# Optimization experiments

Measured on AMD Instinct MI355X. Metric: run time of the kernel, lower is better.

## Reference

```python
import jax, jax.numpy as jnp
import numpy as np

B, C_IN, L = 8, 64, 4096
C_OUT, HEADS = 64, 3
E = 524288
T_DIM = 256
N = B * L
EPS = 1e-5
NEG_SLOPE = 0.2  # PyG GATConv default negative_slope


def setup_inputs() -> dict:
    key = jax.random.key(0)
    ks = jax.random.split(key, 12)
    x = jax.random.normal(ks[0], (B, C_IN, L), jnp.float32)
    time_emb = jax.random.normal(ks[1], (B, T_DIM), jnp.float32)
    edge_index = jax.random.randint(ks[2], (2, E), 0, N, dtype=jnp.int32)
    # GATConv params: lin maps in -> heads*out; att_src/att_dst per head
    W_lin = jax.random.normal(ks[3], (C_IN, HEADS * C_OUT), jnp.float32) / np.sqrt(C_IN)
    att_src = jax.random.normal(ks[4], (1, HEADS, C_OUT), jnp.float32) / np.sqrt(C_OUT)
    att_dst = jax.random.normal(ks[5], (1, HEADS, C_OUT), jnp.float32) / np.sqrt(C_OUT)
    bias = jnp.zeros((C_OUT,), jnp.float32)
    # time projection (computed but unused in the source forward)
    tp_W = jax.random.normal(ks[6], (T_DIM, C_OUT), jnp.float32) / np.sqrt(T_DIM)
    tp_b = jnp.zeros((C_OUT,), jnp.float32)
    # BatchNorm1d affine params (training-mode batch stats)
    gamma = jnp.ones((C_OUT,), jnp.float32)
    beta = jnp.zeros((C_OUT,), jnp.float32)
    return {"x": x, "time_emb": time_emb, "edge_index": edge_index,
            "W_lin": W_lin, "att_src": att_src, "att_dst": att_dst,
            "bias": bias, "tp_W": tp_W, "tp_b": tp_b,
            "gamma": gamma, "beta": beta}


def reference(x, time_emb, edge_index, W_lin, att_src, att_dst, bias, tp_W, tp_b, gamma, beta):
    b, c, l = x.shape
    n = b * l
    # time projection: present in source but its result is never used
    _t = (time_emb @ tp_W + tp_b)[:, :, None]  # [b, C_OUT, 1] (dead)
    h = (x.reshape(-1, c) @ W_lin).reshape(n, HEADS, C_OUT)  # [N,H,C]
    a_src = (h * att_src).sum(-1)  # [N,H]
    a_dst = (h * att_dst).sum(-1)  # [N,H]
    # add self loops (PyG default add_self_loops=True)
    loops = jnp.arange(n, dtype=edge_index.dtype)
    src = jnp.concatenate([edge_index[0], loops])
    dst = jnp.concatenate([edge_index[1], loops])
    e = a_src[src] + a_dst[dst]                        # [E+N, H]
    e = jnp.where(e > 0, e, NEG_SLOPE * e)             # LeakyReLU
    emax = jax.ops.segment_max(e, dst, num_segments=n)  # every node has a self loop
    ex = jnp.exp(e - emax[dst])
    denom = jax.ops.segment_sum(ex, dst, num_segments=n)
    alpha = ex / denom[dst]                            # segment softmax over dst
    msg = alpha[:, :, None] * h[src]                   # [E+N, H, C]
    out = jax.ops.segment_sum(msg, dst, num_segments=n)  # [N,H,C]
    out = out.mean(axis=1) + bias                      # concat=False -> head mean
    # BatchNorm1d (training mode: biased batch stats)
    mu = out.mean(axis=0)
    var = ((out - mu) ** 2).mean(axis=0)
    out = (out - mu) / jnp.sqrt(var + EPS) * gamma + beta
    out = jax.nn.relu(out)
    return out.reshape(b, -1, l)
```

## Files before the change

### kernel.cpp

```cpp
#include <hip/hip_runtime.h>
#include <hip/hip_bf16.h>

#define N_NODES 32768
#define E_EDGES 524288
#define HC 192
#define NEG_SLOPE 0.2f
#define BN_EPS 1e-5f
#define PAD 64

typedef _Float16 f16;
typedef __attribute__((ext_vector_type(8))) _Float16 v8h;
typedef __attribute__((ext_vector_type(4))) float    v4f;

#define GEMM_BLOCKS 512
#define SCAT_BLOCKS 2048
#define FUSED_BLOCKS (GEMM_BLOCKS + SCAT_BLOCKS)

__device__ __forceinline__ float lrelu(float v) { return v > 0.f ? v : NEG_SLOPE * v; }

__device__ __forceinline__ float wave_sum(float v) {
#pragma unroll
    for (int off = 32; off > 0; off >>= 1) v += __shfl_xor(v, off);
    return v;
}
__device__ __forceinline__ float rlane(float v, int l) {
    return __uint_as_float(__builtin_amdgcn_readlane(__float_as_uint(v), l));
}

__global__ __launch_bounds__(256, 2) void k_fused(
        const int* __restrict__ esrc, const int* __restrict__ edst,
        int* __restrict__ cnt, unsigned short* __restrict__ csr_pad,
        const float* __restrict__ x, const float* __restrict__ W,
        const float* __restrict__ att_s, const float* __restrict__ att_d,
        f16* __restrict__ hh, float* __restrict__ a_src, float* __restrict__ a_dst,
        float* __restrict__ gp1, float* __restrict__ gp2) {
    if (blockIdx.x >= GEMM_BLOCKS) {
        int i = (blockIdx.x - GEMM_BLOCKS) * 256 + threadIdx.x;
        int s = esrc[i];
        int d = edst[i];
        int p = atomicAdd(&cnt[d], 1);
        if (p < PAD) csr_pad[d * PAD + p] = (unsigned short)s;
        return;
    }
    if (blockIdx.x == 0) {
        float4 z = make_float4(0.f, 0.f, 0.f, 0.f);
#pragma unroll
        for (int i2 = 0; i2 < 4; i2++) {
            ((float4*)gp1)[threadIdx.x * 4 + i2] = z;
            ((float4*)gp2)[threadIdx.x * 4 + i2] = z;
        }
    }
    const int lane = threadIdx.x & 63;
    const int wid  = (blockIdx.x * 256 + threadIdx.x) >> 6;
    const int q    = lane >> 4;
    const int nl   = lane & 15;
    const int n0   = wid * 16;

    v8h xf0, xf1;
    {
        const float* xr = x + (size_t)(n0 + nl) * 64 + q * 8;
        float4 lo = *(const float4*)(xr);
        float4 hi = *(const float4*)(xr + 4);
        xf0[0] = (f16)lo.x; xf0[1] = (f16)lo.y; xf0[2] = (f16)lo.z; xf0[3] = (f16)lo.w;
        xf0[4] = (f16)hi.x; xf0[5] = (f16)hi.y; xf0[6] = (f16)hi.z; xf0[7] = (f16)hi.w;
        lo = *(const float4*)(xr + 32);
        hi = *(const float4*)(xr + 36);
        xf1[0] = (f16)lo.x; xf1[1] = (f16)lo.y; xf1[2] = (f16)lo.z; xf1[3] = (f16)lo.w;
        xf1[4] = (f16)hi.x; xf1[5] = (f16)hi.y; xf1[6] = (f16)hi.z; xf1[7] = (f16)hi.w;
    }

    float sAcc = 0.f, dAcc = 0.f;
#pragma unroll
    for (int ct = 0; ct < 12; ct++) {
        const int c = ct * 16 + nl;
        v8h wf0, wf1;
#pragma unroll
        for (int j = 0; j < 8; j++) {
            wf0[j] = (f16)W[(q * 8 + j) * HC + c];
            wf1[j] = (f16)W[(32 + q * 8 + j) * HC + c];
        }
        float4 av = *(const float4*)(att_s + ct * 16 + q * 4);
        float4 dv = *(const float4*)(att_d + ct * 16 + q * 4);

        v4f C = {0.f, 0.f, 0.f, 0.f};
        C = __builtin_amdgcn_mfma_f32_16x16x32_f16(wf0, xf0, C, 0, 0, 0);
        C = __builtin_amdgcn_mfma_f32_16x16x32_f16(wf1, xf1, C, 0, 0, 0);

        union { f16 h[4]; unsigned long long u; } pk;
        pk.h[0] = (f16)C[0]; pk.h[1] = (f16)C[1];
        pk.h[2] = (f16)C[2]; pk.h[3] = (f16)C[3];
        *(unsigned long long*)(hh + (size_t)(n0 + nl) * HC + ct * 16 + q * 4) = pk.u;

        sAcc = fmaf(C[0], av.x, sAcc); sAcc = fmaf(C[1], av.y, sAcc);
        sAcc = fmaf(C[2], av.z, sAcc); sAcc = fmaf(C[3], av.w, sAcc);
        dAcc = fmaf(C[0], dv.x, dAcc); dAcc = fmaf(C[1], dv.y, dAcc);
        dAcc = fmaf(C[2], dv.z, dAcc); dAcc = fmaf(C[3], dv.w, dAcc);

        if ((ct & 3) == 3) {
            float s = sAcc; s += __shfl_xor(s, 16); s += __shfl_xor(s, 32);
            float d = dAcc; d += __shfl_xor(d, 16); d += __shfl_xor(d, 32);
            if (lane < 16) {
                a_src[(n0 + lane) * 4 + (ct >> 2)] = s;
                a_dst[(n0 + lane) * 4 + (ct >> 2)] = d;
            }
            sAcc = 0.f; dAcc = 0.f;
        }
    }
}

__global__ __launch_bounds__(256, 4) void k_node(
        const f16* __restrict__ hh,
        const float* __restrict__ a_src,
        const float* __restrict__ a_dst,
        const int* __restrict__ cnt,
        const unsigned short* __restrict__ csr_pad,
        const float* __restrict__ bias,
        float* __restrict__ out_pre,
        float* __restrict__ gp1,
        float* __restrict__ gp2) {
    const int lane = threadIdx.x & 63;
    const int wv = threadIdx.x >> 6;
    const int n = blockIdx.x * 4 + wv;

    int deg = cnt[n]; if (deg > PAD) deg = PAD;
    const unsigned short* __restrict__ row = csr_pad + n * PAD;

    const float ad0 = a_dst[n * 4 + 0], ad1 = a_dst[n * 4 + 1], ad2 = a_dst[n * 4 + 2];

    float ws0 = __expf(lrelu(a_src[n * 4 + 0] + ad0));
    float ws1 = __expf(lrelu(a_src[n * 4 + 1] + ad1));
    float ws2 = __expf(lrelu(a_src[n * 4 + 2] + ad2));
    float den0 = ws0, den1 = ws1, den2 = ws2;
    const f16* hn = hh + (size_t)n * HC;
    float acc0 = ws0 * (float)hn[lane];
    float acc1 = ws1 * (float)hn[64 + lane];
    float acc2 = ws2 * (float)hn[128 + lane];

    int s = 0;
    float w0 = 0.f, w1 = 0.f, w2 = 0.f;
    if (lane < deg) {
        s = (int)row[lane];
        float4 as = ((const float4*)a_src)[s];
        w0 = __expf(lrelu(as.x + ad0));
        w1 = __expf(lrelu(as.y + ad1));
        w2 = __expf(lrelu(as.z + ad2));
    }
    den0 += wave_sum(w0);
    den1 += wave_sum(w1);
    den2 += wave_sum(w2);

    int j = 0;
    for (; j + 8 <= deg; j += 8) {
#pragma unroll
        for (int u = 0; u < 8; u += 4) {
            int s0 = __builtin_amdgcn_readlane(s, j + u);
            int s1 = __builtin_amdgcn_readlane(s, j + u + 1);
            int s2 = __builtin_amdgcn_readlane(s, j + u + 2);
            int s3 = __builtin_amdgcn_readlane(s, j + u + 3);
            const f16* __restrict__ h0 = hh + (size_t)s0 * HC;
            const f16* __restrict__ h1 = hh + (size_t)s1 * HC;
            const f16* __restrict__ h2 = hh + (size_t)s2 * HC;
            const f16* __restrict__ h3 = hh + (size_t)s3 * HC;
            float v00 = (float)h0[lane], v01 = (float)h0[64 + lane], v02 = (float)h0[128 + lane];
            float v10 = (float)h1[lane], v11 = (float)h1[64 + lane], v12 = (float)h1[128 + lane];
            float v20 = (float)h2[lane], v21 = (float)h2[64 + lane], v22 = (float)h2[128 + lane];
            float v30 = (float)h3[lane], v31 = (float)h3[64 + lane], v32 = (float)h3[128 + lane];
            float w00 = rlane(w0, j + u),     w01 = rlane(w1, j + u),     w02 = rlane(w2, j + u);
            float w10 = rlane(w0, j + u + 1), w11 = rlane(w1, j + u + 1), w12 = rlane(w2, j + u + 1);
            float w20 = rlane(w0, j + u + 2), w21 = rlane(w1, j + u + 2), w22 = rlane(w2, j + u + 2);
            float w30 = rlane(w0, j + u + 3), w31 = rlane(w1, j + u + 3), w32 = rlane(w2, j + u + 3);
            acc0 = fmaf(w00, v00, acc0); acc0 = fmaf(w10, v10, acc0);
            acc0 = fmaf(w20, v20, acc0); acc0 = fmaf(w30, v30, acc0);
            acc1 = fmaf(w01, v01, acc1); acc1 = fmaf(w11, v11, acc1);
            acc1 = fmaf(w21, v21, acc1); acc1 = fmaf(w31, v31, acc1);
            acc2 = fmaf(w02, v02, acc2); acc2 = fmaf(w12, v12, acc2);
            acc2 = fmaf(w22, v22, acc2); acc2 = fmaf(w32, v32, acc2);
        }
    }
    for (; j < deg; j++) {
        int sa = __builtin_amdgcn_readlane(s, j);
        const f16* __restrict__ ha = hh + (size_t)sa * HC;
        float wa0 = rlane(w0, j), wa1 = rlane(w1, j), wa2 = rlane(w2, j);
        acc0 = fmaf(wa0, (float)ha[lane], acc0);
        acc1 = fmaf(wa1, (float)ha[64 + lane], acc1);
        acc2 = fmaf(wa2, (float)ha[128 + lane], acc2);
    }

    float outv = (acc0 / den0 + acc1 / den1 + acc2 / den2) * (1.0f / 3.0f) + bias[lane];
    out_pre[n * 64 + lane] = outv;

    __shared__ float ls[4][64], lq[4][64];
    ls[wv][lane] = outv;
    lq[wv][lane] = outv * outv;
    __syncthreads();
    if (threadIdx.x < 64) {
        int t = threadIdx.x;
        float s_ = ls[0][t] + ls[1][t] + ls[2][t] + ls[3][t];
        float q_ = lq[0][t] + lq[1][t] + lq[2][t] + lq[3][t];
        int slice = blockIdx.x & 63;
        atomicAdd(&gp1[slice * 64 + t], s_);
        atomicAdd(&gp2[slice * 64 + t], q_);
    }
}

#define APPLY_BLOCKS 512
__global__ __launch_bounds__(256) void k_apply(const float4* __restrict__ out_pre4,
                                               const float* __restrict__ gp1,
                                               const float* __restrict__ gp2,
                                               const float* __restrict__ gamma,
                                               const float* __restrict__ beta,
                                               float4* __restrict__ out4) {
    __shared__ float sc[64], sh[64];
    if (threadIdx.x < 64) {
        int t = threadIdx.x;
        float s = 0.f, q = 0.f;
        for (int i = 0; i < 64; i++) { s += gp1[i * 64 + t]; q += gp2[i * 64 + t]; }
        const float inv_n = 1.0f / (float)N_NODES;
        float mu = s * inv_n;
        float var = q * inv_n - mu * mu;
        float invstd = 1.0f / sqrtf(var + BN_EPS);
        float scale = invstd * gamma[t];
        sc[t] = scale;
        sh[t] = beta[t] - mu * scale;
    }
    __syncthreads();
    const int total = N_NODES * 64 / 4;
    for (int idx = blockIdx.x * 256 + threadIdx.x; idx < total; idx += APPLY_BLOCKS * 256) {
        int c0 = (idx * 4) & 63;
        float4 v = out_pre4[idx];
        float4 r;
        r.x = fmaxf(v.x * sc[c0 + 0] + sh[c0 + 0], 0.f);
        r.y = fmaxf(v.y * sc[c0 + 1] + sh[c0 + 1], 0.f);
        r.z = fmaxf(v.z * sc[c0 + 2] + sh[c0 + 2], 0.f);
        r.w = fmaxf(v.w * sc[c0 + 3] + sh[c0 + 3], 0.f);
        out4[idx] = r;
    }
}

extern "C" void kernel_launch(void* const* d_in, const int* in_sizes, int n_in,
                              void* d_out, int out_size, void* d_ws, size_t ws_size,
                              hipStream_t stream) {
    const float* x     = (const float*)d_in[0];
    const int*   ei    = (const int*)d_in[2];
    const float* W     = (const float*)d_in[3];
    const float* att_s = (const float*)d_in[4];
    const float* att_d = (const float*)d_in[5];
    const float* bias  = (const float*)d_in[6];
    const float* gamma = (const float*)d_in[9];
    const float* beta  = (const float*)d_in[10];
    float* out = (float*)d_out;

    char* ws = (char*)d_ws;
    size_t off = 0;
    auto alloc = [&](size_t bytes) -> void* {
        void* p = ws + off;
        off += (bytes + 255) & ~(size_t)255;
        return p;
    };
    f16*            hh      = (f16*)alloc((size_t)N_NODES * HC * 2);
    float*          a_src   = (float*)alloc((size_t)N_NODES * 4 * 4);
    float*          a_dst   = (float*)alloc((size_t)N_NODES * 4 * 4);
    int*            cnt     = (int*)alloc((size_t)N_NODES * 4);
    unsigned short* csr_pad = (unsigned short*)alloc((size_t)N_NODES * PAD * 2);
    float*          out_pre = (float*)alloc((size_t)N_NODES * 64 * 4);
    float*          gp1     = (float*)alloc(64 * 64 * 4);
    float*          gp2     = (float*)alloc(64 * 64 * 4);

    hipMemsetAsync(cnt, 0, (size_t)N_NODES * 4, stream);

    k_fused<<<FUSED_BLOCKS, 256, 0, stream>>>(
        ei, ei + E_EDGES, cnt, csr_pad,
        x, W, att_s, att_d, hh, a_src, a_dst, gp1, gp2);
    k_node<<<N_NODES / 4, 256, 0, stream>>>(hh, a_src, a_dst, cnt, csr_pad, bias,
                                            out_pre, gp1, gp2);
    k_apply<<<APPLY_BLOCKS, 256, 0, stream>>>((const float4*)out_pre, gp1, gp2,
                                              gamma, beta, (float4*)out);
}
```

Before: 147.8 us.

## Interleave GEMM and scatter blocks, persist node blocks over 8 nodes each

The fused kernel now interleaves GEMM blocks among scatter blocks (one GEMM block in every five) instead of placing all GEMM blocks first, and raises its occupancy hint from 2 to 4 blocks per SM. The node kernel now launches 1024 blocks that each loop over 8 groups of 4 nodes. Each wave accumulates its BatchNorm partial sums in registers, so the per-block shared-memory reduction and atomics run once per 32 nodes rather than per 4. The aim is to balance the mix of work across CUs and cut reduction and atomic overhead, at the cost of less parallelism in the node kernel and possible register pressure from the higher occupancy hint.

```diff
diff --git a/kernel.cpp b/kernel.cpp
--- a/kernel.cpp
+++ b/kernel.cpp
@@ -16,6 +16,9 @@
 #define SCAT_BLOCKS 2048
 #define FUSED_BLOCKS (GEMM_BLOCKS + SCAT_BLOCKS)
 
+#define NODE_BLOCKS 1024
+#define APPLY_BLOCKS 512
+
 __device__ __forceinline__ float lrelu(float v) { return v > 0.f ? v : NEG_SLOPE * v; }
 
 __device__ __forceinline__ float wave_sum(float v) {
@@ -27,22 +30,26 @@
     return __uint_as_float(__builtin_amdgcn_readlane(__float_as_uint(v), l));
 }
 
-__global__ __launch_bounds__(256, 2) void k_fused(
+__global__ __launch_bounds__(256, 4) void k_fused(
         const int* __restrict__ esrc, const int* __restrict__ edst,
         int* __restrict__ cnt, unsigned short* __restrict__ csr_pad,
         const float* __restrict__ x, const float* __restrict__ W,
         const float* __restrict__ att_s, const float* __restrict__ att_d,
         f16* __restrict__ hh, float* __restrict__ a_src, float* __restrict__ a_dst,
         float* __restrict__ gp1, float* __restrict__ gp2) {
-    if (blockIdx.x >= GEMM_BLOCKS) {
-        int i = (blockIdx.x - GEMM_BLOCKS) * 256 + threadIdx.x;
+    const int bid = blockIdx.x;
+    if ((bid % 5) != 2) {
+        const int g = bid % 5;
+        const int sid = (bid / 5) * 4 + g - (g > 2 ? 1 : 0);
+        int i = sid * 256 + threadIdx.x;
         int s = esrc[i];
         int d = edst[i];
         int p = atomicAdd(&cnt[d], 1);
         if (p < PAD) csr_pad[d * PAD + p] = (unsigned short)s;
         return;
     }
-    if (blockIdx.x == 0) {
+    const int gid = bid / 5;
+    if (gid == 0) {
         float4 z = make_float4(0.f, 0.f, 0.f, 0.f);
 #pragma unroll
         for (int i2 = 0; i2 < 4; i2++) {
@@ -51,7 +58,7 @@
         }
     }
     const int lane = threadIdx.x & 63;
-    const int wid  = (blockIdx.x * 256 + threadIdx.x) >> 6;
+    const int wid  = (gid * 256 + threadIdx.x) >> 6;
     const int q    = lane >> 4;
     const int nl   = lane & 15;
     const int n0   = wid * 16;
@@ -120,78 +127,87 @@
         float* __restrict__ gp2) {
     const int lane = threadIdx.x & 63;
     const int wv = threadIdx.x >> 6;
-    const int n = blockIdx.x * 4 + wv;
-
-    int deg = cnt[n]; if (deg > PAD) deg = PAD;
-    const unsigned short* __restrict__ row = csr_pad + n * PAD;
-
-    const float ad0 = a_dst[n * 4 + 0], ad1 = a_dst[n * 4 + 1], ad2 = a_dst[n * 4 + 2];
-
-    float ws0 = __expf(lrelu(a_src[n * 4 + 0] + ad0));
-    float ws1 = __expf(lrelu(a_src[n * 4 + 1] + ad1));
-    float ws2 = __expf(lrelu(a_src[n * 4 + 2] + ad2));
-    float den0 = ws0, den1 = ws1, den2 = ws2;
-    const f16* hn = hh + (size_t)n * HC;
-    float acc0 = ws0 * (float)hn[lane];
-    float acc1 = ws1 * (float)hn[64 + lane];
-    float acc2 = ws2 * (float)hn[128 + lane];
-
-    int s = 0;
-    float w0 = 0.f, w1 = 0.f, w2 = 0.f;
-    if (lane < deg) {
-        s = (int)row[lane];
-        float4 as = ((const float4*)a_src)[s];
-        w0 = __expf(lrelu(as.x + ad0));
-        w1 = __expf(lrelu(as.y + ad1));
-        w2 = __expf(lrelu(as.z + ad2));
-    }
-    den0 += wave_sum(w0);
-    den1 += wave_sum(w1);
-    den2 += wave_sum(w2);
-
-    int j = 0;
-    for (; j + 8 <= deg; j += 8) {
-#pragma unroll
-        for (int u = 0; u < 8; u += 4) {
-            int s0 = __builtin_amdgcn_readlane(s, j + u);
-            int s1 = __builtin_amdgcn_readlane(s, j + u + 1);
-            int s2 = __builtin_amdgcn_readlane(s, j + u + 2);
-            int s3 = __builtin_amdgcn_readlane(s, j + u + 3);
-            const f16* __restrict__ h0 = hh + (size_t)s0 * HC;
-            const f16* __restrict__ h1 = hh + (size_t)s1 * HC;
-            const f16* __restrict__ h2 = hh + (size_t)s2 * HC;
-            const f16* __restrict__ h3 = hh + (size_t)s3 * HC;
-            float v00 = (float)h0[lane], v01 = (float)h0[64 + lane], v02 = (float)h0[128 + lane];
-            float v10 = (float)h1[lane], v11 = (float)h1[64 + lane], v12 = (float)h1[128 + lane];
-            float v20 = (float)h2[lane], v21 = (float)h2[64 + lane], v22 = (float)h2[128 + lane];
-            float v30 = (float)h3[lane], v31 = (float)h3[64 + lane], v32 = (float)h3[128 + lane];
-            float w00 = rlane(w0, j + u),     w01 = rlane(w1, j + u),     w02 = rlane(w2, j + u);
-            float w10 = rlane(w0, j + u + 1), w11 = rlane(w1, j + u + 1), w12 = rlane(w2, j + u + 1);
-            float w20 = rlane(w0, j + u + 2), w21 = rlane(w1, j + u + 2), w22 = rlane(w2, j + u + 2);
-            float w30 = rlane(w0, j + u + 3), w31 = rlane(w1, j + u + 3), w32 = rlane(w2, j + u + 3);
-            acc0 = fmaf(w00, v00, acc0); acc0 = fmaf(w10, v10, acc0);
-            acc0 = fmaf(w20, v20, acc0); acc0 = fmaf(w30, v30, acc0);
-            acc1 = fmaf(w01, v01, acc1); acc1 = fmaf(w11, v11, acc1);
-            acc1 = fmaf(w21, v21, acc1); acc1 = fmaf(w31, v31, acc1);
-            acc2 = fmaf(w02, v02, acc2); acc2 = fmaf(w12, v12, acc2);
-            acc2 = fmaf(w22, v22, acc2); acc2 = fmaf(w32, v32, acc2);
-        }
-    }
-    for (; j < deg; j++) {
-        int sa = __builtin_amdgcn_readlane(s, j);
-        const f16* __restrict__ ha = hh + (size_t)sa * HC;
-        float wa0 = rlane(w0, j), wa1 = rlane(w1, j), wa2 = rlane(w2, j);
-        acc0 = fmaf(wa0, (float)ha[lane], acc0);
-        acc1 = fmaf(wa1, (float)ha[64 + lane], acc1);
-        acc2 = fmaf(wa2, (float)ha[128 + lane], acc2);
-    }
-
-    float outv = (acc0 / den0 + acc1 / den1 + acc2 / den2) * (1.0f / 3.0f) + bias[lane];
-    out_pre[n * 64 + lane] = outv;
+    const float bias_l = bias[lane];
+
+    float bn_s = 0.f, bn_q = 0.f;
+
+#pragma unroll 1
+    for (int it = 0; it < 8; it++) {
+        const int n = blockIdx.x * 32 + it * 4 + wv;
+
+        int deg = cnt[n]; if (deg > PAD) deg = PAD;
+        const unsigned short* __restrict__ row = csr_pad + n * PAD;
+
+        const float ad0 = a_dst[n * 4 + 0], ad1 = a_dst[n * 4 + 1], ad2 = a_dst[n * 4 + 2];
+
+        float ws0 = __expf(lrelu(a_src[n * 4 + 0] + ad0));
+        float ws1 = __expf(lrelu(a_src[n * 4 + 1] + ad1));
+        float ws2 = __expf(lrelu(a_src[n * 4 + 2] + ad2));
+        float den0 = ws0, den1 = ws1, den2 = ws2;
+        const f16* hn = hh + (size_t)n * HC;
+        float acc0 = ws0 * (float)hn[lane];
+        float acc1 = ws1 * (float)hn[64 + lane];
+        float acc2 = ws2 * (float)hn[128 + lane];
+
+        int s = 0;
+        float w0 = 0.f, w1 = 0.f, w2 = 0.f;
+        if (lane < deg) {
+            s = (int)row[lane];
+            float4 as = ((const float4*)a_src)[s];
+            w0 = __expf(lrelu(as.x + ad0));
+            w1 = __expf(lrelu(as.y + ad1));
+            w2 = __expf(lrelu(as.z + ad2));
+        }
+        den0 += wave_sum(w0);
+        den1 += wave_sum(w1);
+        den2 += wave_sum(w2);
+
+        int j = 0;
+        for (; j + 8 <= deg; j += 8) {
+#pragma unroll
+            for (int u = 0; u < 8; u += 4) {
+                int s0 = __builtin_amdgcn_readlane(s, j + u);
+                int s1 = __builtin_amdgcn_readlane(s, j + u + 1);
+                int s2 = __builtin_amdgcn_readlane(s, j + u + 2);
+                int s3 = __builtin_amdgcn_readlane(s, j + u + 3);
+                const f16* __restrict__ h0 = hh + (size_t)s0 * HC;
+                const f16* __restrict__ h1 = hh + (size_t)s1 * HC;
+                const f16* __restrict__ h2 = hh + (size_t)s2 * HC;
+                const f16* __restrict__ h3 = hh + (size_t)s3 * HC;
+                float v00 = (float)h0[lane], v01 = (float)h0[64 + lane], v02 = (float)h0[128 + lane];
+                float v10 = (float)h1[lane], v11 = (float)h1[64 + lane], v12 = (float)h1[128 + lane];
+                float v20 = (float)h2[lane], v21 = (float)h2[64 + lane], v22 = (float)h2[128 + lane];
+                float v30 = (float)h3[lane], v31 = (float)h3[64 + lane], v32 = (float)h3[128 + lane];
+                float w00 = rlane(w0, j + u),     w01 = rlane(w1, j + u),     w02 = rlane(w2, j + u);
+                float w10 = rlane(w0, j + u + 1), w11 = rlane(w1, j + u + 1), w12 = rlane(w2, j + u + 1);
+                float w20 = rlane(w0, j + u + 2), w21 = rlane(w1, j + u + 2), w22 = rlane(w2, j + u + 2);
+                float w30 = rlane(w0, j + u + 3), w31 = rlane(w1, j + u + 3), w32 = rlane(w2, j + u + 3);
+                acc0 = fmaf(w00, v00, acc0); acc0 = fmaf(w10, v10, acc0);
+                acc0 = fmaf(w20, v20, acc0); acc0 = fmaf(w30, v30, acc0);
+                acc1 = fmaf(w01, v01, acc1); acc1 = fmaf(w11, v11, acc1);
+                acc1 = fmaf(w21, v21, acc1); acc1 = fmaf(w31, v31, acc1);
+                acc2 = fmaf(w02, v02, acc2); acc2 = fmaf(w12, v12, acc2);
+                acc2 = fmaf(w22, v22, acc2); acc2 = fmaf(w32, v32, acc2);
+            }
+        }
+        for (; j < deg; j++) {
+            int sa = __builtin_amdgcn_readlane(s, j);
+            const f16* __restrict__ ha = hh + (size_t)sa * HC;
+            float wa0 = rlane(w0, j), wa1 = rlane(w1, j), wa2 = rlane(w2, j);
+            acc0 = fmaf(wa0, (float)ha[lane], acc0);
+            acc1 = fmaf(wa1, (float)ha[64 + lane], acc1);
+            acc2 = fmaf(wa2, (float)ha[128 + lane], acc2);
+        }
+
+        float outv = (acc0 / den0 + acc1 / den1 + acc2 / den2) * (1.0f / 3.0f) + bias_l;
+        out_pre[n * 64 + lane] = outv;
+        bn_s += outv;
+        bn_q += outv * outv;
+    }
 
     __shared__ float ls[4][64], lq[4][64];
-    ls[wv][lane] = outv;
-    lq[wv][lane] = outv * outv;
+    ls[wv][lane] = bn_s;
+    lq[wv][lane] = bn_q;
     __syncthreads();
     if (threadIdx.x < 64) {
         int t = threadIdx.x;
@@ -203,7 +219,6 @@
     }
 }
 
-#define APPLY_BLOCKS 512
 __global__ __launch_bounds__(256) void k_apply(const float4* __restrict__ out_pre4,
                                                const float* __restrict__ gp1,
                                                const float* __restrict__ gp2,
@@ -271,7 +286,7 @@
     k_fused<<<FUSED_BLOCKS, 256, 0, stream>>>(
         ei, ei + E_EDGES, cnt, csr_pad,
         x, W, att_s, att_d, hh, a_src, a_dst, gp1, gp2);
-    k_node<<<N_NODES / 4, 256, 0, stream>>>(hh, a_src, a_dst, cnt, csr_pad, bias,
+    k_node<<<NODE_BLOCKS, 256, 0, stream>>>(hh, a_src, a_dst, cnt, csr_pad, bias,
                                             out_pre, gp1, gp2);
     k_apply<<<APPLY_BLOCKS, 256, 0, stream>>>((const float4*)out_pre, gp1, gp2,
                                               gamma, beta, (float4*)out);
```

New measurement: 161.3 us. 9.2% more time.
